# Optimization experiments

Hardware: AMD Instinct MI355X
Metric: run time of the kernel (lower is better)

Reference implementation:

```python
import jax, jax.numpy as jnp
import numpy as np

N_EMBD = 16
HEAD_SIZE = 64
B, T = 8, 4096


def setup_inputs() -> dict:
    key = jax.random.key(0)
    k_x, k_q, k_k, k_v = jax.random.split(key, 4)
    # Uniform(0,1) keeps QK^T scores strictly positive so the fractional
    # power (-1/16) is well-defined (negative base would NaN, same as torch).
    x = jax.random.uniform(k_x, (B, T, N_EMBD), dtype=jnp.float32)
    Wq = jax.random.uniform(k_q, (N_EMBD, HEAD_SIZE), dtype=jnp.float32) * 0.25
    Wk = jax.random.uniform(k_k, (N_EMBD, HEAD_SIZE), dtype=jnp.float32) * 0.25
    Wv = jax.random.uniform(k_v, (N_EMBD, HEAD_SIZE), dtype=jnp.float32) * 0.25
    return {"x": x, "Wq": Wq, "Wk": Wk, "Wv": Wv}


def reference(x, Wq, Wk, Wv):
    features_dim = x.shape[-1]  # n_embd = 16
    q = x @ Wq                                   # [B, T, H]
    k = x @ Wk                                   # [B, T, H]
    scores = jnp.einsum('bth,bsh->bts', q, k)    # [B, T, T]
    scores = scores ** (-1.0 / features_dim)     # elementwise power, NOT a scale
    attn = jax.nn.softmax(scores, axis=1)        # softmax over QUERY axis (dim=1)
    v = x @ Wk                                   # faithful to source: uses keys_matrix, not Wv
    return jnp.einsum('bts,bsh->bth', attn, v)   # [B, T, H]
```

## Files before the change

kernel.cpp:

```cpp
#include <hip/hip_runtime.h>
#include <hip/hip_bf16.h>

#define BB 8
#define TT 4096
#define EE 16
#define HH 64
#define ZT 16
#define NS 8

typedef __attribute__((ext_vector_type(8))) __bf16 bf16x8;
typedef __attribute__((ext_vector_type(4))) __bf16 bf16x4;
typedef __attribute__((ext_vector_type(4))) float f32x4;
typedef __attribute__((ext_vector_type(16))) float f32x16;

static __device__ __forceinline__ float exp_pow16(float d) {
    float L = __builtin_amdgcn_logf(d);
    float r = __builtin_fmaf(L, 2.72889e-6f, -1.536072e-4f);
    r = __builtin_fmaf(L, r, 4.946584e-3f);
    r = __builtin_fmaf(L, r, -0.11735442f);
    r = __builtin_fmaf(L, r, 2.71784054f);
    return r;
}

__global__ __launch_bounds__(256) void proj_kernel(
        const float* __restrict__ x, const float* __restrict__ Wq,
        const float* __restrict__ Wk,
        __bf16* __restrict__ Yb, __bf16* __restrict__ xb,
        float* __restrict__ Dsum) {
    __shared__ float Ms[16][16];
    __shared__ float xs[16][16];
    int tid = threadIdx.x;
    size_t gid = (size_t)blockIdx.x * 256 + tid;
    if (gid < (size_t)BB * TT / 4)
        ((float4*)Dsum)[gid] = (float4){0.f, 0.f, 0.f, 0.f};
    int i = tid >> 4, j = tid & 15;
    float m = 0.f;
#pragma unroll 8
    for (int h = 0; h < HH; ++h) m += Wq[i * HH + h] * Wk[j * HH + h];
    Ms[i][j] = m;
    int row0 = blockIdx.x * 16;
    xs[i][j] = x[(size_t)(row0 + i) * EE + j];
    __syncthreads();
    float y = 0.f;
#pragma unroll
    for (int k = 0; k < EE; ++k) y += xs[i][k] * Ms[k][j];
    size_t idx = (size_t)(row0 + i) * EE + j;
    Yb[idx] = (__bf16)y;
    xb[idx] = (__bf16)xs[i][j];
}

__global__ __launch_bounds__(256) void colsum_mfma(
        const __bf16* __restrict__ Yb, const __bf16* __restrict__ xb,
        float* __restrict__ Dsum) {
    int lane = threadIdx.x & 63;
    int w = threadIdx.x >> 6;
    int wl = lane & 31;
    int hi = lane >> 5;
    int b = blockIdx.y;
    int z = blockIdx.z;
    int s0 = blockIdx.x * 256 + w * 64;

    const __bf16* xbb = xb + (size_t)b * TT * EE;
    const __bf16* Ybb = Yb + (size_t)b * TT * EE;

    bf16x8 bx[2];
#pragma unroll
    for (int sg = 0; sg < 2; ++sg)
        bx[sg] = *(const bf16x8*)(xbb + (size_t)(s0 + sg * 32 + wl) * EE + hi * 8);

    const __bf16* gya = Ybb + (size_t)wl * EE + hi * 8;

    const int TL = TT / ZT;
    int t0 = z * TL, tend = t0 + TL;

    float csum[2] = {0.f, 0.f};

    auto BODY = [&](bf16x8 ya) {
#pragma unroll
        for (int sg = 0; sg < 2; ++sg) {
            f32x16 c = {};
            c = __builtin_amdgcn_mfma_f32_32x32x16_bf16(ya, bx[sg], c, 0, 0, 0);
#pragma unroll
            for (int r = 0; r < 16; ++r) {
                float L = __builtin_amdgcn_logf(c[r]);
                float p = __builtin_fmaf(L, 2.72889e-6f, -1.536072e-4f);
                p = __builtin_fmaf(L, p, 4.946584e-3f);
                p = __builtin_fmaf(L, p, -0.11735442f);
                csum[sg] = __builtin_fmaf(L, p, csum[sg]);
            }
        }
    };

    bf16x8 yaA, yaB;
    yaA = *(const bf16x8*)(gya + (size_t)t0 * EE);
    for (int t = t0; t < tend; t += 64) {
        yaB = *(const bf16x8*)(gya + (size_t)(t + 32) * EE);
        BODY(yaA);
        int tn = (t + 64 < tend) ? (t + 64) : t0;
        yaA = *(const bf16x8*)(gya + (size_t)tn * EE);
        BODY(yaB);
    }

#pragma unroll
    for (int sg = 0; sg < 2; ++sg) {
        float r = csum[sg];
        r += __shfl_xor(r, 32, 64);
        if (lane < 32)
            atomicAdd(&Dsum[(size_t)b * TT + s0 + sg * 32 + wl],
                      r + 256.0f * 2.71784054f);
    }
}

__global__ __launch_bounds__(256) void xd_kernel(
        const __bf16* __restrict__ xb, const float* __restrict__ Dsum,
        __bf16* __restrict__ xDT, float* __restrict__ Z) {
    __shared__ float Rs[64];
    __shared__ __bf16 tt[16][68];
    int b = blockIdx.y;
    int s0 = blockIdx.x * 64;
    int tid = threadIdx.x;
    size_t zi = ((size_t)b * gridDim.x + blockIdx.x) * 256 + tid;
    ((float4*)Z)[zi] = (float4){0.f, 0.f, 0.f, 0.f};
    if (tid < 64)
        Rs[tid] = 1.0f / Dsum[(size_t)b * TT + s0 + tid];
    __syncthreads();
    int sl = tid & 63, eg = tid >> 6;
    bf16x4 v = *(const bf16x4*)(xb + ((size_t)b * TT + s0 + sl) * EE + eg * 4);
    float r = Rs[sl];
#pragma unroll
    for (int i = 0; i < 4; ++i) tt[eg * 4 + i][sl] = (__bf16)((float)v[i] * r);
    __syncthreads();
    int e = tid >> 4, sc = tid & 15;
    *(bf16x4*)(xDT + ((size_t)b * EE + e) * TT + s0 + sc * 4) = *(const bf16x4*)&tt[e][sc * 4];
}

__global__ __launch_bounds__(256) void out_mfma(
        const __bf16* __restrict__ Yb, const __bf16* __restrict__ xb,
        const __bf16* __restrict__ xDT, float* __restrict__ Z) {
    __shared__ __bf16 Etile[2][4][32 * 36];

    int lane = threadIdx.x & 63;
    int w = threadIdx.x >> 6;
    int wl = lane & 31;
    int hi = lane >> 5;
    int quad = lane >> 4;
    int l15 = lane & 15;
    int b = blockIdx.y;
    int z = blockIdx.z;
    int t0 = blockIdx.x * 128 + w * 32;

    const __bf16* xbb = xb + (size_t)b * TT * EE;
    const __bf16* Ybb = Yb + (size_t)b * TT * EE;
    const __bf16* xdb = xDT + (size_t)b * EE * TT;

    bf16x8 yf = *(const bf16x8*)(Ybb + (size_t)(t0 + wl) * EE + hi * 8);

    f32x4 acc[2] = {{0.f, 0.f, 0.f, 0.f}, {0.f, 0.f, 0.f, 0.f}};

    const __bf16* gaf = xbb + (size_t)wl * EE + hi * 8;
    const __bf16* gxd = xdb + (size_t)l15 * TT + quad * 8;

    const int SL = TT / NS;
    int s0z = z * SL, send = s0z + SL;

    auto STAGE = [&](bf16x8 af, int p) {
        f32x16 c = {};
        c = __builtin_amdgcn_mfma_f32_32x32x16_bf16(af, yf, c, 0, 0, 0);
#pragma unroll
        for (int g = 0; g < 4; ++g) {
            bf16x4 e;
#pragma unroll
            for (int r = 0; r < 4; ++r)
                e[r] = (__bf16)exp_pow16(c[g * 4 + r]);
            *(bf16x4*)&Etile[p][w][wl * 36 + g * 8 + hi * 4] = e;
        }
    };
    auto PV = [&](bf16x8& bxd, int p) {
#pragma unroll
        for (int h2 = 0; h2 < 2; ++h2) {
            bf16x8 aE = *(const bf16x8*)&Etile[p][w][(h2 * 16 + l15) * 36 + quad * 8];
            acc[h2] = __builtin_amdgcn_mfma_f32_16x16x32_bf16(aE, bxd, acc[h2], 0, 0, 0);
        }
    };

    bf16x8 afA, afB, bxdA, bxdB;
    afA = *(const bf16x8*)(gaf + (size_t)s0z * EE);
    bxdA = *(const bf16x8*)(gxd + s0z);
    STAGE(afA, 0);
    for (int s = s0z; s < send; s += 64) {
        afB = *(const bf16x8*)(gaf + (size_t)(s + 32) * EE);
        bxdB = *(const bf16x8*)(gxd + (s + 32));
        STAGE(afB, 1);
        PV(bxdA, 0);
        int sn = s + 64;
        if (sn < send) {
            afA = *(const bf16x8*)(gaf + (size_t)sn * EE);
            bxdA = *(const bf16x8*)(gxd + sn);
            STAGE(afA, 0);
        }
        PV(bxdB, 1);
    }

    float* zp = Z + ((size_t)b * TT + t0) * EE;
#pragma unroll
    for (int h2 = 0; h2 < 2; ++h2)
#pragma unroll
        for (int r = 0; r < 4; ++r)
            atomicAdd(&zp[(size_t)(h2 * 16 + quad * 4 + r) * EE + l15], acc[h2][r]);
}

__global__ __launch_bounds__(256) void zout_kernel(
        const float* __restrict__ Z, const float* __restrict__ Wk,
        float* __restrict__ out) {
    __shared__ float zs[64][16];
    int b = blockIdx.y;
    int t0 = blockIdx.x * 64;
    int tid = threadIdx.x;
    ((float4*)zs)[tid] = ((const float4*)(Z + ((size_t)b * TT + t0) * EE))[tid];
    __syncthreads();
    int h = tid & 63, tg = tid >> 6;
    float wcol[16];
#pragma unroll
    for (int e = 0; e < EE; ++e) wcol[e] = Wk[e * HH + h];
    float* ob = out + ((size_t)b * TT + t0) * HH + h;
#pragma unroll
    for (int k = 0; k < 16; ++k) {
        int tl = tg * 16 + k;
        float o = 0.f;
#pragma unroll
        for (int e = 0; e < EE; ++e) o = __builtin_fmaf(zs[tl][e], wcol[e], o);
        ob[(size_t)tl * HH] = o;
    }
}

extern "C" void kernel_launch(void* const* d_in, const int* in_sizes, int n_in,
                              void* d_out, int out_size, void* d_ws, size_t ws_size,
                              hipStream_t stream) {
    const float* x  = (const float*)d_in[0];
    const float* Wq = (const float*)d_in[1];
    const float* Wk = (const float*)d_in[2];

    const size_t NE16 = (size_t)BB * TT * EE;
    char* wp = (char*)d_ws;
    __bf16* Yb   = (__bf16*)wp;  wp += NE16 * 2;
    __bf16* xbb  = (__bf16*)wp;  wp += NE16 * 2;
    __bf16* xDT  = (__bf16*)wp;  wp += NE16 * 2;
    float*  Dsum = (float*)wp;   wp += (size_t)BB * TT * 4;
    float*  Zws  = (float*)wp;

    float* out = (float*)d_out;

    proj_kernel<<<BB * TT / 16, 256, 0, stream>>>(x, Wq, Wk, Yb, xbb, Dsum);
    colsum_mfma<<<dim3(TT / 256, BB, ZT), 256, 0, stream>>>(Yb, xbb, Dsum);
    xd_kernel<<<dim3(TT / 64, BB), 256, 0, stream>>>(xbb, Dsum, xDT, Zws);
    out_mfma<<<dim3(TT / 128, BB, NS), 256, 0, stream>>>(Yb, xbb, xDT, Zws);
    zout_kernel<<<dim3(TT / 64, BB), 256, 0, stream>>>(Zws, Wk, out);
}
```

Before: 141.4 us.

## Keep exp tile in registers via permlane32 swap instead of LDS round-trip

The out_mfma kernel no longer stages the exponentiated score tile through shared memory. It packs the values to bf16 in registers, rearranges them across half-waves with v_permlane32_swap so the 32x32 MFMA output layout becomes the A-operand layout, and runs the PV product as two 32x32x16 MFMAs into one accumulator. This removes LDS writes and reads and their latency from the inner loop. In exchange it relies on gfx950-specific inline asm, computes 32 output columns of which only 16 are valid (half the PV MFMA work is wasted), and changes the final atomic scatter pattern.

```diff
diff --git a/kernel.cpp b/kernel.cpp
--- a/kernel.cpp
+++ b/kernel.cpp
@@ -12,6 +12,7 @@
 typedef __attribute__((ext_vector_type(4))) __bf16 bf16x4;
 typedef __attribute__((ext_vector_type(4))) float f32x4;
 typedef __attribute__((ext_vector_type(16))) float f32x16;
+typedef __attribute__((ext_vector_type(4))) unsigned u32x4;
 
 static __device__ __forceinline__ float exp_pow16(float d) {
     float L = __builtin_amdgcn_logf(d);
@@ -137,14 +138,10 @@
 __global__ __launch_bounds__(256) void out_mfma(
         const __bf16* __restrict__ Yb, const __bf16* __restrict__ xb,
         const __bf16* __restrict__ xDT, float* __restrict__ Z) {
-    __shared__ __bf16 Etile[2][4][32 * 36];
-
     int lane = threadIdx.x & 63;
     int w = threadIdx.x >> 6;
     int wl = lane & 31;
     int hi = lane >> 5;
-    int quad = lane >> 4;
-    int l15 = lane & 15;
     int b = blockIdx.y;
     int z = blockIdx.z;
     int t0 = blockIdx.x * 128 + w * 32;
@@ -155,58 +152,67 @@
 
     bf16x8 yf = *(const bf16x8*)(Ybb + (size_t)(t0 + wl) * EE + hi * 8);
 
-    f32x4 acc[2] = {{0.f, 0.f, 0.f, 0.f}, {0.f, 0.f, 0.f, 0.f}};
+    f32x16 acc = {};
 
     const __bf16* gaf = xbb + (size_t)wl * EE + hi * 8;
-    const __bf16* gxd = xdb + (size_t)l15 * TT + quad * 8;
+    const __bf16* gxd = xdb + (size_t)(wl & 15) * TT + hi * 8;
 
     const int SL = TT / NS;
     int s0z = z * SL, send = s0z + SL;
 
-    auto STAGE = [&](bf16x8 af, int p) {
+    auto BODY = [&](bf16x8 af, bf16x8 bxd1, bf16x8 bxd2) {
         f32x16 c = {};
         c = __builtin_amdgcn_mfma_f32_32x32x16_bf16(af, yf, c, 0, 0, 0);
-#pragma unroll
-        for (int g = 0; g < 4; ++g) {
-            bf16x4 e;
-#pragma unroll
-            for (int r = 0; r < 4; ++r)
-                e[r] = (__bf16)exp_pow16(c[g * 4 + r]);
-            *(bf16x4*)&Etile[p][w][wl * 36 + g * 8 + hi * 4] = e;
+        float e[16];
+#pragma unroll
+        for (int r = 0; r < 16; ++r) e[r] = exp_pow16(c[r]);
+        unsigned Wd[8];
+#pragma unroll
+        for (int q = 0; q < 4; ++q)
+#pragma unroll
+            for (int h = 0; h < 2; ++h)
+                asm("v_cvt_pk_bf16_f32 %0, %1, %2"
+                    : "=v"(Wd[q * 2 + h])
+                    : "v"(e[4 * q + 2 * h]), "v"(e[4 * q + 2 * h + 1]));
+#pragma unroll
+        for (int h = 0; h < 2; ++h) {
+            asm volatile("v_permlane32_swap_b32 %0, %1"
+                         : "+v"(Wd[0 + h]), "+v"(Wd[2 + h]));
+            asm volatile("v_permlane32_swap_b32 %0, %1"
+                         : "+v"(Wd[4 + h]), "+v"(Wd[6 + h]));
         }
+        u32x4 f1 = {Wd[0], Wd[1], Wd[2], Wd[3]};
+        u32x4 f2 = {Wd[4], Wd[5], Wd[6], Wd[7]};
+        bf16x8 a1, a2;
+        __builtin_memcpy(&a1, &f1, 16);
+        __builtin_memcpy(&a2, &f2, 16);
+        acc = __builtin_amdgcn_mfma_f32_32x32x16_bf16(a1, bxd1, acc, 0, 0, 0);
+        acc = __builtin_amdgcn_mfma_f32_32x32x16_bf16(a2, bxd2, acc, 0, 0, 0);
     };
-    auto PV = [&](bf16x8& bxd, int p) {
-#pragma unroll
-        for (int h2 = 0; h2 < 2; ++h2) {
-            bf16x8 aE = *(const bf16x8*)&Etile[p][w][(h2 * 16 + l15) * 36 + quad * 8];
-            acc[h2] = __builtin_amdgcn_mfma_f32_16x16x32_bf16(aE, bxd, acc[h2], 0, 0, 0);
+    auto LOADF = [&](bf16x8& af, bf16x8& b1, bf16x8& b2, int s) {
+        af = *(const bf16x8*)(gaf + (size_t)s * EE);
+        b1 = *(const bf16x8*)(gxd + s);
+        b2 = *(const bf16x8*)(gxd + s + 16);
+    };
+
+    bf16x8 afA, b1A, b2A, afB, b1B, b2B;
+    LOADF(afA, b1A, b2A, s0z);
+    for (int s = s0z; s < send; s += 64) {
+        LOADF(afB, b1B, b2B, s + 32);
+        BODY(afA, b1A, b2A);
+        int sn = (s + 64 < send) ? (s + 64) : s0z;
+        LOADF(afA, b1A, b2A, sn);
+        BODY(afB, b1B, b2B);
+    }
+
+    float* zp = Z + ((size_t)b * TT + t0) * EE;
+    if (wl < 16) {
+#pragma unroll
+        for (int r = 0; r < 16; ++r) {
+            int t = (r & 3) + 8 * (r >> 2) + 4 * hi;
+            atomicAdd(&zp[(size_t)t * EE + wl], acc[r]);
         }
-    };
-
-    bf16x8 afA, afB, bxdA, bxdB;
-    afA = *(const bf16x8*)(gaf + (size_t)s0z * EE);
-    bxdA = *(const bf16x8*)(gxd + s0z);
-    STAGE(afA, 0);
-    for (int s = s0z; s < send; s += 64) {
-        afB = *(const bf16x8*)(gaf + (size_t)(s + 32) * EE);
-        bxdB = *(const bf16x8*)(gxd + (s + 32));
-        STAGE(afB, 1);
-        PV(bxdA, 0);
-        int sn = s + 64;
-        if (sn < send) {
-            afA = *(const bf16x8*)(gaf + (size_t)sn * EE);
-            bxdA = *(const bf16x8*)(gxd + sn);
-            STAGE(afA, 0);
-        }
-        PV(bxdB, 1);
-    }
-
-    float* zp = Z + ((size_t)b * TT + t0) * EE;
-#pragma unroll
-    for (int h2 = 0; h2 < 2; ++h2)
-#pragma unroll
-        for (int r = 0; r < 4; ++r)
-            atomicAdd(&zp[(size_t)(h2 * 16 + quad * 4 + r) * EE + l15], acc[h2][r]);
+    }
 }
 
 __global__ __launch_bounds__(256) void zout_kernel(
```

Result: slower. 148.2 us (+4.8%).

## Fuse xd and zout kernels via last-block atomic counters

Applied to the files above, without the earlier changes.

Removes the separate xd_kernel and zout_kernel launches. Their work now runs in the last finishing block of colsum_mfma and out_mfma, chosen through per-tile atomic counters. Zeroing of Z and of the counters moves into proj_kernel. This cuts two kernel launches and their inter-kernel gaps. In exchange, the tail work runs serially in a few blocks, uses atomic reads for memory visibility, and writes xDT transposed without coalescing.

```diff
diff --git a/kernel.cpp b/kernel.cpp
--- a/kernel.cpp
+++ b/kernel.cpp
@@ -26,13 +26,18 @@
         const float* __restrict__ x, const float* __restrict__ Wq,
         const float* __restrict__ Wk,
         __bf16* __restrict__ Yb, __bf16* __restrict__ xb,
-        float* __restrict__ Dsum) {
+        float* __restrict__ Dsum, float* __restrict__ Z,
+        int* __restrict__ cnt) {
     __shared__ float Ms[16][16];
     __shared__ float xs[16][16];
     int tid = threadIdx.x;
     size_t gid = (size_t)blockIdx.x * 256 + tid;
     if (gid < (size_t)BB * TT / 4)
         ((float4*)Dsum)[gid] = (float4){0.f, 0.f, 0.f, 0.f};
+    if (gid < (size_t)BB * TT * EE / 4)
+        ((float4*)Z)[gid] = (float4){0.f, 0.f, 0.f, 0.f};
+    if (blockIdx.x == 0)
+        for (int i = tid; i < 384; i += 256) cnt[i] = 0;
     int i = tid >> 4, j = tid & 15;
     float m = 0.f;
 #pragma unroll 8
@@ -51,7 +56,9 @@
 
 __global__ __launch_bounds__(256) void colsum_mfma(
         const __bf16* __restrict__ Yb, const __bf16* __restrict__ xb,
-        float* __restrict__ Dsum) {
+        float* __restrict__ Dsum, __bf16* __restrict__ xDT,
+        int* __restrict__ cnt1) {
+    __shared__ int isLast;
     int lane = threadIdx.x & 63;
     int w = threadIdx.x >> 6;
     int wl = lane & 31;
@@ -109,35 +116,38 @@
             atomicAdd(&Dsum[(size_t)b * TT + s0 + sg * 32 + wl],
                       r + 256.0f * 2.71784054f);
     }
-}
-
-__global__ __launch_bounds__(256) void xd_kernel(
-        const __bf16* __restrict__ xb, const float* __restrict__ Dsum,
-        __bf16* __restrict__ xDT, float* __restrict__ Z) {
-    __shared__ float Rs[64];
-    __shared__ __bf16 tt[16][68];
-    int b = blockIdx.y;
-    int s0 = blockIdx.x * 64;
+
+    __syncthreads();
+    if (threadIdx.x == 0) {
+        int old = atomicAdd(&cnt1[b * (TT / 256) + blockIdx.x], 1);
+        isLast = (old == ZT - 1);
+    }
+    __syncthreads();
+    if (!isLast) return;
+
     int tid = threadIdx.x;
-    size_t zi = ((size_t)b * gridDim.x + blockIdx.x) * 256 + tid;
-    ((float4*)Z)[zi] = (float4){0.f, 0.f, 0.f, 0.f};
-    if (tid < 64)
-        Rs[tid] = 1.0f / Dsum[(size_t)b * TT + s0 + tid];
-    __syncthreads();
-    int sl = tid & 63, eg = tid >> 6;
-    bf16x4 v = *(const bf16x4*)(xb + ((size_t)b * TT + s0 + sl) * EE + eg * 4);
-    float r = Rs[sl];
-#pragma unroll
-    for (int i = 0; i < 4; ++i) tt[eg * 4 + i][sl] = (__bf16)((float)v[i] * r);
-    __syncthreads();
-    int e = tid >> 4, sc = tid & 15;
-    *(bf16x4*)(xDT + ((size_t)b * EE + e) * TT + s0 + sc * 4) = *(const bf16x4*)&tt[e][sc * 4];
+    int s = blockIdx.x * 256 + tid;
+    float d = atomicAdd(&Dsum[(size_t)b * TT + s], 0.0f);
+    float rv = 1.0f / d;
+    const __bf16* xr = xbb + (size_t)s * EE;
+    bf16x8 x0 = *(const bf16x8*)xr;
+    bf16x8 x1 = *(const bf16x8*)(xr + 8);
+    __bf16* xdp = xDT + (size_t)b * EE * TT + s;
+#pragma unroll
+    for (int e = 0; e < 8; ++e)
+        xdp[(size_t)e * TT] = (__bf16)((float)x0[e] * rv);
+#pragma unroll
+    for (int e = 0; e < 8; ++e)
+        xdp[(size_t)(e + 8) * TT] = (__bf16)((float)x1[e] * rv);
 }
 
 __global__ __launch_bounds__(256) void out_mfma(
         const __bf16* __restrict__ Yb, const __bf16* __restrict__ xb,
-        const __bf16* __restrict__ xDT, float* __restrict__ Z) {
+        const __bf16* __restrict__ xDT, float* __restrict__ Z,
+        const float* __restrict__ Wk, float* __restrict__ out,
+        int* __restrict__ cnt2) {
     __shared__ __bf16 Etile[2][4][32 * 36];
+    __shared__ int isLast;
 
     int lane = threadIdx.x & 63;
     int w = threadIdx.x >> 6;
@@ -207,28 +217,34 @@
 #pragma unroll
         for (int r = 0; r < 4; ++r)
             atomicAdd(&zp[(size_t)(h2 * 16 + quad * 4 + r) * EE + l15], acc[h2][r]);
-}
-
-__global__ __launch_bounds__(256) void zout_kernel(
-        const float* __restrict__ Z, const float* __restrict__ Wk,
-        float* __restrict__ out) {
-    __shared__ float zs[64][16];
-    int b = blockIdx.y;
-    int t0 = blockIdx.x * 64;
+
+    __syncthreads();
+    if (threadIdx.x == 0) {
+        int old = atomicAdd(&cnt2[b * (TT / 128) + blockIdx.x], 1);
+        isLast = (old == NS - 1);
+    }
+    __syncthreads();
+    if (!isLast) return;
+
     int tid = threadIdx.x;
-    ((float4*)zs)[tid] = ((const float4*)(Z + ((size_t)b * TT + t0) * EE))[tid];
+    int t0b = blockIdx.x * 128;
+    float* zs = (float*)&Etile[0][0][0];
+    float* Zbase = Z + ((size_t)b * TT + t0b) * EE;
+    for (int i = tid; i < 128 * 16; i += 256)
+        zs[i] = atomicAdd(&Zbase[i], 0.0f);
     __syncthreads();
     int h = tid & 63, tg = tid >> 6;
     float wcol[16];
 #pragma unroll
     for (int e = 0; e < EE; ++e) wcol[e] = Wk[e * HH + h];
-    float* ob = out + ((size_t)b * TT + t0) * HH + h;
-#pragma unroll
-    for (int k = 0; k < 16; ++k) {
-        int tl = tg * 16 + k;
+    float* ob = out + ((size_t)b * TT + t0b) * HH + h;
+#pragma unroll
+    for (int k = 0; k < 32; ++k) {
+        int tl = tg * 32 + k;
         float o = 0.f;
 #pragma unroll
-        for (int e = 0; e < EE; ++e) o = __builtin_fmaf(zs[tl][e], wcol[e], o);
+        for (int e = 0; e < EE; ++e)
+            o = __builtin_fmaf(zs[tl * 16 + e], wcol[e], o);
         ob[(size_t)tl * HH] = o;
     }
 }
@@ -246,13 +262,14 @@
     __bf16* xbb  = (__bf16*)wp;  wp += NE16 * 2;
     __bf16* xDT  = (__bf16*)wp;  wp += NE16 * 2;
     float*  Dsum = (float*)wp;   wp += (size_t)BB * TT * 4;
-    float*  Zws  = (float*)wp;
+    float*  Zws  = (float*)wp;   wp += NE16 * 4;
+    int*    cnt  = (int*)wp;
+    int*    cnt1 = cnt;
+    int*    cnt2 = cnt + 128;
 
     float* out = (float*)d_out;
 
-    proj_kernel<<<BB * TT / 16, 256, 0, stream>>>(x, Wq, Wk, Yb, xbb, Dsum);
-    colsum_mfma<<<dim3(TT / 256, BB, ZT), 256, 0, stream>>>(Yb, xbb, Dsum);
-    xd_kernel<<<dim3(TT / 64, BB), 256, 0, stream>>>(xbb, Dsum, xDT, Zws);
-    out_mfma<<<dim3(TT / 128, BB, NS), 256, 0, stream>>>(Yb, xbb, xDT, Zws);
-    zout_kernel<<<dim3(TT / 64, BB), 256, 0, stream>>>(Zws, Wk, out);
-}
+    proj_kernel<<<BB * TT / 16, 256, 0, stream>>>(x, Wq, Wk, Yb, xbb, Dsum, Zws, cnt);
+    colsum_mfma<<<dim3(TT / 256, BB, ZT), 256, 0, stream>>>(Yb, xbb, Dsum, xDT, cnt1);
+    out_mfma<<<dim3(TT / 128, BB, NS), 256, 0, stream>>>(Yb, xbb, xDT, Zws, Wk, out, cnt2);
+}
```

Result: no change. 143.2 us (+1.3%).
